# Kernel tuning notes

Measured on AMD Instinct MI355X. Metric: run time of the kernel, lower is better.

Reference implementation:

```python
import jax, jax.numpy as jnp
import numpy as np

PC_RANGE = (-50.0, -50.0, -4.0, 50.0, 50.0, 4.0)
IMG_H, IMG_W = 256.0, 704.0
EPS = 1e-5


def _bilinear_sample(feat, u, v):
    # feat [H,W,C]; u,v [M] in [0,1]; matches F.grid_sample(align_corners=False, padding_mode='zeros')
    H, W, _ = feat.shape
    x = u * W - 0.5
    y = v * H - 0.5
    x0 = jnp.floor(x)
    y0 = jnp.floor(y)
    dx = (x - x0)[:, None]
    dy = (y - y0)[:, None]
    x0 = x0.astype(jnp.int32)
    y0 = y0.astype(jnp.int32)

    def g(xi, yi):
        inb = ((xi >= 0) & (xi < W) & (yi >= 0) & (yi < H)).astype(feat.dtype)[:, None]
        return feat[jnp.clip(yi, 0, H - 1), jnp.clip(xi, 0, W - 1)] * inb

    return (g(x0, y0) * (1 - dx) * (1 - dy) + g(x0 + 1, y0) * dx * (1 - dy)
            + g(x0, y0 + 1) * (1 - dx) * dy + g(x0 + 1, y0 + 1) * dx * dy)


def _conv1x1(t, w, b):
    return jnp.einsum('bchw,oc->bohw', t, w) + b[None, :, None, None]


def _inorm(t, eps=1e-5):
    # InstanceNorm2d (affine=False): normalize per (b, c) over spatial dims
    m = t.mean(axis=(2, 3), keepdims=True)
    var = t.var(axis=(2, 3), keepdims=True)
    return (t - m) * jax.lax.rsqrt(var + eps)


def _forward(feat, lidar2img, bev_pos, pe_w1, pe_b1, pe_w2, pe_b2, pe_w3, pe_b3,
             c1_w, c1_b, c2_w, c2_b, c3_w, c3_b):
    B, N, C, Hf, Wf = feat.shape
    _, P, Hb, Wb, _ = bev_pos.shape
    Q = Hb * Wb
    lo = jnp.asarray(PC_RANGE[:3], feat.dtype)
    hi = jnp.asarray(PC_RANGE[3:], feat.dtype)
    # 'b p h w d -> b (h w) p d', then scale normalized coords into pc_range
    ref01 = jnp.transpose(bev_pos, (0, 2, 3, 1, 4)).reshape(B, Q, P, 3)
    ref = ref01 * (hi - lo) + lo
    # project through per-camera lidar2img (homogeneous)
    pts = jnp.concatenate([ref, jnp.ones_like(ref[..., :1])], axis=-1)  # [B,Q,P,4]
    cam = jnp.einsum('bnij,bqpj->bnqpi', lidar2img, pts)                # [B,N,Q,P,4]
    homo = cam[..., 2]
    z = jnp.maximum(homo, EPS)
    u = cam[..., 0] / z / IMG_W
    v = cam[..., 1] / z / IMG_H
    valid = ((homo > EPS) & (u > 0.0) & (u < 1.0) & (v > 0.0) & (v < 1.0)).astype(feat.dtype)
    # bilinear gather per camera; feats to channel-last ('b n (g c) h w -> (b g) n h w c', G=1)
    fmap = jnp.transpose(feat, (0, 1, 3, 4, 2)).reshape(B * N, Hf, Wf, C)
    samp = jax.vmap(_bilinear_sample)(fmap, u.reshape(B * N, Q * P), v.reshape(B * N, Q * P))
    samp = samp.reshape(B, N, Q, P, C) * valid[..., None]
    samp = samp.sum(axis=1)  # sum over cameras -> [B,Q,P,C]
    # PositionalEncodingMap(3 -> 256 -> 256 -> 128) on normalized reference points
    pe = jax.nn.relu(ref01 @ pe_w1 + pe_b1)
    pe = jax.nn.relu(pe @ pe_w2 + pe_b2)
    pe = pe @ pe_w3 + pe_b3
    samp = samp + pe
    # 'b (h w) g p c -> b (p g c) h w' with g=1
    x = jnp.transpose(samp.reshape(B, Hb, Wb, P, C), (0, 3, 4, 1, 2)).reshape(B, P * C, Hb, Wb)
    gelu = lambda t: jax.nn.gelu(t, approximate=False)
    x = gelu(_inorm(_conv1x1(x, c1_w, c1_b)))
    x = gelu(_inorm(_conv1x1(x, c2_w, c2_b)))
    x = _conv1x1(x, c3_w, c3_b)
    return x


def setup_inputs() -> dict:
    key = jax.random.key(0)
    ks = jax.random.split(key, 16)
    B, N, C, Hf, Wf = 1, 6, 128, 32, 88
    P, Hb, Wb = 4, 160, 160
    E = 128
    MID = 256
    s = 0.02
    return {
        'feat': jax.random.normal(ks[0], (B, N, C, Hf, Wf), jnp.float32),
        'lidar2img': jax.random.normal(ks[1], (B, N, 4, 4), jnp.float32),
        'bev_pos': jax.random.uniform(ks[2], (B, P, Hb, Wb, 3), jnp.float32),
        'pe_w1': jax.random.normal(ks[3], (3, MID), jnp.float32) * s,
        'pe_b1': jnp.zeros((MID,), jnp.float32),
        'pe_w2': jax.random.normal(ks[4], (MID, MID), jnp.float32) * s,
        'pe_b2': jnp.zeros((MID,), jnp.float32),
        'pe_w3': jax.random.normal(ks[5], (MID, E), jnp.float32) * s,
        'pe_b3': jnp.zeros((E,), jnp.float32),
        'c1_w': jax.random.normal(ks[6], (4 * E, P * 128), jnp.float32) * s,
        'c1_b': jnp.zeros((4 * E,), jnp.float32),
        'c2_w': jax.random.normal(ks[7], (E, 4 * E), jnp.float32) * s,
        'c2_b': jnp.zeros((E,), jnp.float32),
        'c3_w': jax.random.normal(ks[8], (E, E), jnp.float32) * s,
        'c3_b': jnp.zeros((E,), jnp.float32),
    }


def reference(feat, lidar2img, bev_pos, pe_w1, pe_b1, pe_w2, pe_b2, pe_w3, pe_b3,
              c1_w, c1_b, c2_w, c2_b, c3_w, c3_b):
    return _forward(feat, lidar2img, bev_pos, pe_w1, pe_b1, pe_w2, pe_b2, pe_w3, pe_b3,
                    c1_w, c1_b, c2_w, c2_b, c3_w, c3_b)
```

## Files before the change

### kernel.cpp

```cpp
#include <hip/hip_runtime.h>
#include <cstdint>
#include <cstddef>

using frag8 = __attribute__((ext_vector_type(8))) short;
using f32x4 = __attribute__((ext_vector_type(4))) float;

__device__ __forceinline__ float b2f_bits(unsigned short u) {
    union { uint32_t u32; float f; } x; x.u32 = ((uint32_t)u) << 16; return x.f;
}
__device__ __forceinline__ float b2f_lo(uint32_t pk) {
    return __builtin_bit_cast(float, pk << 16);
}
__device__ __forceinline__ float b2f_hi(uint32_t pk) {
    return __builtin_bit_cast(float, pk & 0xffff0000u);
}
__device__ __forceinline__ unsigned short f2b(float f) {
    uint32_t u = __builtin_bit_cast(uint32_t, f);
    uint32_t r = (u + 0x7fffu + ((u >> 16) & 1u)) >> 16;
    return (unsigned short)r;
}

#define HF 32
#define WFEAT 88
#define NCAM 6
#define NPT 102400
#define BM 128
#define BN 128
#define BK 64

__global__ void k_transpose_feat(const float* __restrict__ feat,
                                 unsigned short* __restrict__ featT) {
    int idx = blockIdx.x * 256 + threadIdx.x;
    if (idx >= NCAM * 128 * HF * WFEAT) return;
    int c = idx & 127;
    int rest = idx >> 7;
    int x = rest % WFEAT; rest /= WFEAT;
    int y = rest % HF;
    int n = rest / HF;
    featT[idx] = f2b(feat[((n * 128 + c) * HF + y) * WFEAT + x]);
}

__global__ void k_transpose_w(const float* __restrict__ w,
                              unsigned short* __restrict__ wt, int R, int C) {
    int idx = blockIdx.x * 256 + threadIdx.x;
    if (idx >= R * C) return;
    int r = idx / C, c = idx - r * C;
    wt[c * R + r] = f2b(w[idx]);
}

__global__ void k_cast(const float* __restrict__ w, unsigned short* __restrict__ wb, int n) {
    int idx = blockIdx.x * 256 + threadIdx.x;
    if (idx < n) wb[idx] = f2b(w[idx]);
}

__global__ __launch_bounds__(256) void k_project(const float* __restrict__ l2i,
                                                 const float* __restrict__ bev,
                                                 int* __restrict__ poff,
                                                 float4* __restrict__ pwts) {
    int idx = blockIdx.x * 256 + threadIdx.x;
    if (idx >= NCAM * NPT) return;
    int n = idx / NPT, pt = idx - n * NPT;
    int q = pt >> 2, p = pt & 3;
    int h = q / 160, w = q - h * 160;
    const float* bv = bev + ((p * 160 + h) * 160 + w) * 3;
    float rx = bv[0] * 100.f - 50.f;
    float ry = bv[1] * 100.f - 50.f;
    float rz = bv[2] * 8.f - 4.f;
    const float* M = l2i + n * 16;
    float c0   = M[0] * rx + M[1] * ry + M[2]  * rz + M[3];
    float c1v  = M[4] * rx + M[5] * ry + M[6]  * rz + M[7];
    float homo = M[8] * rx + M[9] * ry + M[10] * rz + M[11];
    float z = fmaxf(homo, 1e-5f);
    float u = c0 / z / 704.0f;
    float v = c1v / z / 256.0f;
    if (!(homo > 1e-5f && u > 0.f && u < 1.f && v > 0.f && v < 1.f)) {
        poff[idx] = -1;
        return;
    }
    float fx = u * (float)WFEAT - 0.5f;
    float fy = v * (float)HF - 0.5f;
    float fx0 = floorf(fx), fy0 = floorf(fy);
    float dx = fx - fx0, dy = fy - fy0;
    int x0 = (int)fx0, y0 = (int)fy0;
    float wxa = (x0 < 0) ? dx : 1.f - dx;
    float wxb = (x0 >= 0 && x0 < WFEAT - 1) ? dx : 0.f;
    float wya = (y0 < 0) ? dy : 1.f - dy;
    float wyb = (y0 >= 0 && y0 < HF - 1) ? dy : 0.f;
    int bx = max(x0, 0), by = max(y0, 0);
    poff[idx] = ((n * HF + by) * WFEAT + bx) << 7;
    pwts[idx] = make_float4(wxa * wya, wxb * wya, wxa * wyb, wxb * wyb);
}

__global__ __launch_bounds__(256) void k_sample2(const unsigned short* __restrict__ featT,
                                                 const int* __restrict__ poff,
                                                 const float4* __restrict__ pwts,
                                                 unsigned short* __restrict__ samp) {
    int pt = blockIdx.x * 4 + (threadIdx.x >> 6);
    int lane = threadIdx.x & 63;
    int c2 = lane * 2;
    int offs[NCAM];
    float4 ww[NCAM];
    #pragma unroll
    for (int n = 0; n < NCAM; ++n) offs[n] = poff[n * NPT + pt];
    #pragma unroll
    for (int n = 0; n < NCAM; ++n) ww[n] = pwts[n * NPT + pt];
    float acc0 = 0.f, acc1 = 0.f;
    #pragma unroll
    for (int n = 0; n < NCAM; ++n) {
        if (offs[n] >= 0) {
            const unsigned short* base = featT + offs[n] + c2;
            uint32_t p00 = *(const uint32_t*)(base);
            uint32_t p01 = *(const uint32_t*)(base + 128);
            uint32_t p10 = *(const uint32_t*)(base + WFEAT * 128);
            uint32_t p11 = *(const uint32_t*)(base + WFEAT * 128 + 128);
            float4 w = ww[n];
            acc0 += w.x * b2f_lo(p00) + w.y * b2f_lo(p01) + w.z * b2f_lo(p10) + w.w * b2f_lo(p11);
            acc1 += w.x * b2f_hi(p00) + w.y * b2f_hi(p01) + w.z * b2f_hi(p10) + w.w * b2f_hi(p11);
        }
    }
    uint32_t outpk = (uint32_t)f2b(acc0) | ((uint32_t)f2b(acc1) << 16);
    *(uint32_t*)(samp + (size_t)pt * 128 + c2) = outpk;
}

__global__ __launch_bounds__(256) void k_pe1(const float* __restrict__ bev,
                                             const float* __restrict__ w1,
                                             const float* __restrict__ b1,
                                             unsigned short* __restrict__ H1) {
    int idx = blockIdx.x * 256 + threadIdx.x;
    int m = idx >> 6;
    int o4 = (idx & 63) * 4;
    int q = m >> 2, p = m & 3;
    int h = q / 160, w = q - h * 160;
    const float* bv = bev + ((p * 160 + h) * 160 + w) * 3;
    float cx = bv[0], cy = bv[1], cz = bv[2];
    float4 a0 = *(const float4*)(w1 + o4);
    float4 a1 = *(const float4*)(w1 + 256 + o4);
    float4 a2 = *(const float4*)(w1 + 512 + o4);
    float4 bb = *(const float4*)(b1 + o4);
    ushort4 o;
    o.x = f2b(fmaxf(cx * a0.x + cy * a1.x + cz * a2.x + bb.x, 0.f));
    o.y = f2b(fmaxf(cx * a0.y + cy * a1.y + cz * a2.y + bb.y, 0.f));
    o.z = f2b(fmaxf(cx * a0.z + cy * a1.z + cz * a2.z + bb.z, 0.f));
    o.w = f2b(fmaxf(cx * a0.w + cy * a1.w + cz * a2.w + bb.w, 0.f));
    *(ushort4*)(H1 + (size_t)m * 256 + o4) = o;
}

__device__ __forceinline__ void stage_tile(const unsigned short* __restrict__ g, int ld,
                                           unsigned short* lds, int wave, int lane) {
    #pragma unroll
    for (int j = 0; j < 4; ++j) {
        int idx = wave * 256 + j * 64 + lane;
        int r = idx >> 3;
        int cs = idx & 7;
        int cl = cs ^ (r & 7);
        __builtin_amdgcn_global_load_lds(
            (const __attribute__((address_space(1))) void*)(g + (size_t)r * ld + cl * 8),
            (__attribute__((address_space(3))) void*)(lds + wave * 2048 + j * 512),
            16, 0, 0);
    }
}

__device__ __forceinline__ frag8 frag_read(const unsigned short* lds, int row, int chunk) {
    return *(const frag8*)(lds + row * 64 + ((chunk ^ (row & 7)) << 3));
}

__device__ __forceinline__ void mma_tile(const unsigned short* As, const unsigned short* Bs,
                                         int wm, int wn, int lane, f32x4 (&acc)[4][4]) {
    int lm = lane & 15, lq = lane >> 4;
    #pragma unroll
    for (int kk = 0; kk < 2; ++kk) {
        frag8 a[4], b[4];
        #pragma unroll
        for (int t = 0; t < 4; ++t) a[t] = frag_read(As, wm * 64 + t * 16 + lm, kk * 4 + lq);
        #pragma unroll
        for (int t = 0; t < 4; ++t) b[t] = frag_read(Bs, wn * 64 + t * 16 + lm, kk * 4 + lq);
        #pragma unroll
        for (int tm = 0; tm < 4; ++tm)
            #pragma unroll
            for (int tn = 0; tn < 4; ++tn)
                acc[tm][tn] = __builtin_amdgcn_mfma_f32_16x16x32_bf16(a[tm], b[tn], acc[tm][tn], 0, 0, 0);
    }
}

__global__ __launch_bounds__(256) void k_gemm_pe2(const unsigned short* __restrict__ A,
                                                  const unsigned short* __restrict__ Bt,
                                                  const float* __restrict__ bias,
                                                  unsigned short* __restrict__ H2) {
    __shared__ unsigned short As[BM * BK], Bs[BN * BK];
    int lane = threadIdx.x & 63, wave = threadIdx.x >> 6;
    int wm = wave >> 1, wn = wave & 1;
    int m0 = blockIdx.x * BM, n0 = blockIdx.y * BN;
    f32x4 acc[4][4] = {};
    for (int kt = 0; kt < 4; ++kt) {
        stage_tile(A + (size_t)m0 * 256 + kt * BK, 256, As, wave, lane);
        stage_tile(Bt + (size_t)n0 * 256 + kt * BK, 256, Bs, wave, lane);
        __syncthreads();
        mma_tile(As, Bs, wm, wn, lane, acc);
        __syncthreads();
    }
    int lm = lane & 15, lq = lane >> 4;
    #pragma unroll
    for (int tn = 0; tn < 4; ++tn) {
        int n = n0 + wn * 64 + tn * 16 + lm;
        float bn = bias[n];
        #pragma unroll
        for (int tm = 0; tm < 4; ++tm) {
            int mb = m0 + wm * 64 + tm * 16 + lq * 4;
            #pragma unroll
            for (int rr = 0; rr < 4; ++rr)
                H2[(size_t)(mb + rr) * 256 + n] = f2b(fmaxf(acc[tm][tn][rr] + bn, 0.f));
        }
    }
}

__global__ __launch_bounds__(256) void k_gemm_pe3(const unsigned short* __restrict__ A,
                                                  const unsigned short* __restrict__ Bt,
                                                  const float* __restrict__ bias,
                                                  const unsigned short* __restrict__ samp,
                                                  unsigned short* __restrict__ X) {
    __shared__ unsigned short As[BM * BK], Bs[BN * BK];
    int lane = threadIdx.x & 63, wave = threadIdx.x >> 6;
    int wm = wave >> 1, wn = wave & 1;
    int m0 = blockIdx.x * BM;
    f32x4 acc[4][4] = {};
    for (int kt = 0; kt < 4; ++kt) {
        stage_tile(A + (size_t)m0 * 256 + kt * BK, 256, As, wave, lane);
        stage_tile(Bt + (size_t)kt * BK, 256, Bs, wave, lane);
        __syncthreads();
        mma_tile(As, Bs, wm, wn, lane, acc);
        __syncthreads();
    }
    int lm = lane & 15, lq = lane >> 4;
    #pragma unroll
    for (int tn = 0; tn < 4; ++tn) {
        int n = wn * 64 + tn * 16 + lm;
        float bn = bias[n];
        #pragma unroll
        for (int tm = 0; tm < 4; ++tm) {
            int mb = m0 + wm * 64 + tm * 16 + lq * 4;
            #pragma unroll
            for (int rr = 0; rr < 4; ++rr) {
                size_t off = (size_t)(mb + rr) * 128 + n;
                X[off] = f2b(acc[tm][tn][rr] + bn + b2f_bits(samp[off]));
            }
        }
    }
}

template <int K, bool STATS>
__global__ __launch_bounds__(256) void k_gemm_conv(const unsigned short* __restrict__ A,
                                                   const unsigned short* __restrict__ Bt,
                                                   const float* __restrict__ bias,
                                                   unsigned short* __restrict__ Y, int ldY,
                                                   float* __restrict__ st, int C) {
    __shared__ unsigned short As[BM * BK], Bs[BN * BK];
    int lane = threadIdx.x & 63, wave = threadIdx.x >> 6;
    int wm = wave >> 1, wn = wave & 1;
    int m0 = blockIdx.x * BM, n0 = blockIdx.y * BN;
    f32x4 acc[4][4] = {};
    for (int kt = 0; kt < K / BK; ++kt) {
        stage_tile(A + (size_t)m0 * K + kt * BK, K, As, wave, lane);
        stage_tile(Bt + (size_t)n0 * K + kt * BK, K, Bs, wave, lane);
        __syncthreads();
        mma_tile(As, Bs, wm, wn, lane, acc);
        __syncthreads();
    }
    int lm = lane & 15, lq = lane >> 4;
    #pragma unroll
    for (int tn = 0; tn < 4; ++tn) {
        int n = n0 + wn * 64 + tn * 16 + lm;
        float bn = bias[n];
        float s1 = 0.f, s2 = 0.f;
        #pragma unroll
        for (int tm = 0; tm < 4; ++tm) {
            int mb = m0 + wm * 64 + tm * 16 + lq * 4;
            #pragma unroll
            for (int rr = 0; rr < 4; ++rr) {
                float v = acc[tm][tn][rr] + bn;
                Y[(size_t)(mb + rr) * ldY + n] = f2b(v);
                if (STATS) { s1 += v; s2 += v * v; }
            }
        }
        if (STATS) {
            s1 += __shfl_xor(s1, 16); s1 += __shfl_xor(s1, 32);
            s2 += __shfl_xor(s2, 16); s2 += __shfl_xor(s2, 32);
            if (lq == 0) { atomicAdd(&st[n], s1); atomicAdd(&st[C + n], s2); }
        }
    }
}

__global__ __launch_bounds__(256) void k_gemm_conv3(const unsigned short* __restrict__ A,
                                                    const unsigned short* __restrict__ Bt,
                                                    const float* __restrict__ bias,
                                                    float* __restrict__ out) {
    __shared__ unsigned short As[BM * BK], Bs[BN * BK];
    int lane = threadIdx.x & 63, wave = threadIdx.x >> 6;
    int wm = wave >> 1, wn = wave & 1;
    int m0 = blockIdx.x * BM;
    f32x4 acc[4][4] = {};
    for (int kt = 0; kt < 2; ++kt) {
        stage_tile(A + (size_t)m0 * 128 + kt * BK, 128, As, wave, lane);
        stage_tile(Bt + (size_t)kt * BK, 128, Bs, wave, lane);
        __syncthreads();
        mma_tile(As, Bs, wm, wn, lane, acc);
        __syncthreads();
    }
    int lm = lane & 15, lq = lane >> 4;
    #pragma unroll
    for (int tn = 0; tn < 4; ++tn) {
        int n = wn * 64 + tn * 16 + lm;
        float bn = bias[n];
        #pragma unroll
        for (int tm = 0; tm < 4; ++tm) {
            int mb = m0 + wm * 64 + tm * 16 + lq * 4;
            float4 pk;
            pk.x = acc[tm][tn][0] + bn;
            pk.y = acc[tm][tn][1] + bn;
            pk.z = acc[tm][tn][2] + bn;
            pk.w = acc[tm][tn][3] + bn;
            *(float4*)(out + (size_t)n * 25600 + mb) = pk;
        }
    }
}

__global__ void k_finalize(const float* __restrict__ st, float* __restrict__ ms,
                           int C, float inv_n) {
    int c = blockIdx.x * 256 + threadIdx.x;
    if (c >= C) return;
    float mean = st[c] * inv_n;
    float var = st[C + c] * inv_n - mean * mean;
    ms[c] = mean;
    ms[C + c] = rsqrtf(var + 1e-5f);
}

__global__ void k_normgelu8(const unsigned short* __restrict__ Y, const float* __restrict__ ms,
                            unsigned short* __restrict__ X2, int Cmask, int C, int total8) {
    int i8 = blockIdx.x * 256 + threadIdx.x;
    if (i8 >= total8) return;
    int e0 = i8 * 8;
    int c = e0 & Cmask;
    uint4 y = *(const uint4*)(Y + e0);
    const float is2 = 0.70710678118654752f;
    unsigned int yw[4] = {y.x, y.y, y.z, y.w};
    unsigned int ow[4];
    #pragma unroll
    for (int j = 0; j < 4; ++j) {
        float2 mu = *(const float2*)(ms + c + j * 2);
        float2 rs = *(const float2*)(ms + C + c + j * 2);
        float v0 = (b2f_bits((unsigned short)(yw[j] & 0xffffu)) - mu.x) * rs.x;
        float v1 = (b2f_bits((unsigned short)(yw[j] >> 16)) - mu.y) * rs.y;
        float g0 = 0.5f * v0 * (1.f + erff(v0 * is2));
        float g1 = 0.5f * v1 * (1.f + erff(v1 * is2));
        ow[j] = (uint32_t)f2b(g0) | ((uint32_t)f2b(g1) << 16);
    }
    *(uint4*)(X2 + e0) = make_uint4(ow[0], ow[1], ow[2], ow[3]);
}

extern "C" void kernel_launch(void* const* d_in, const int* in_sizes, int n_in,
                              void* d_out, int out_size, void* d_ws, size_t ws_size,
                              hipStream_t stream) {
    (void)in_sizes; (void)n_in; (void)out_size; (void)ws_size;
    const float* feat = (const float*)d_in[0];
    const float* l2i  = (const float*)d_in[1];
    const float* bev  = (const float*)d_in[2];
    const float* pw1  = (const float*)d_in[3];
    const float* pb1  = (const float*)d_in[4];
    const float* pw2  = (const float*)d_in[5];
    const float* pb2  = (const float*)d_in[6];
    const float* pw3  = (const float*)d_in[7];
    const float* pb3  = (const float*)d_in[8];
    const float* c1w  = (const float*)d_in[9];
    const float* c1b  = (const float*)d_in[10];
    const float* c2w  = (const float*)d_in[11];
    const float* c2b  = (const float*)d_in[12];
    const float* c3w  = (const float*)d_in[13];
    const float* c3b  = (const float*)d_in[14];
    float* outp = (float*)d_out;
    char* ws = (char*)d_ws;

    unsigned short* featT = (unsigned short*)(ws + 0);
    unsigned short* W2Tb  = (unsigned short*)(ws + 4348416);
    unsigned short* W3Tb  = (unsigned short*)(ws + 4479488);
    unsigned short* C1Wb  = (unsigned short*)(ws + 4545024);
    unsigned short* C2Wb  = (unsigned short*)(ws + 5069312);
    unsigned short* C3Wb  = (unsigned short*)(ws + 5200384);
    float* stats          = (float*)(ws + 5233152);
    int*    poff          = (int*)(ws + 5243392);
    float4* pwts          = (float4*)(ws + 7700992);
    char* BUF1 = ws + 17531392;
    char* BUF2 = ws + 69960192;
    char* BUF3 = ws + 122388992;

    float* st512 = stats;
    float* ms512 = stats + 1024;
    float* st128 = stats + 2048;
    float* ms128 = stats + 2304;

    unsigned short* H1   = (unsigned short*)BUF1;
    unsigned short* H2   = (unsigned short*)BUF2;
    unsigned short* samp = (unsigned short*)BUF3;
    unsigned short* X    = (unsigned short*)BUF1;
    unsigned short* Y1   = (unsigned short*)BUF2;
    unsigned short* X2   = (unsigned short*)BUF3;
    unsigned short* Y2   = (unsigned short*)BUF1;
    unsigned short* X3   = (unsigned short*)(BUF1 + 6553600);

    k_transpose_feat<<<8448, 256, 0, stream>>>(feat, featT);
    k_transpose_w<<<256, 256, 0, stream>>>(pw2, W2Tb, 256, 256);
    k_transpose_w<<<128, 256, 0, stream>>>(pw3, W3Tb, 256, 128);
    k_cast<<<1024, 256, 0, stream>>>(c1w, C1Wb, 262144);
    k_cast<<<256, 256, 0, stream>>>(c2w, C2Wb, 65536);
    k_cast<<<64, 256, 0, stream>>>(c3w, C3Wb, 16384);
    hipMemsetAsync(stats, 0, 10240, stream);

    k_project<<<2400, 256, 0, stream>>>(l2i, bev, poff, pwts);
    k_sample2<<<25600, 256, 0, stream>>>(featT, poff, pwts, samp);

    k_pe1<<<25600, 256, 0, stream>>>(bev, pw1, pb1, H1);
    k_gemm_pe2<<<dim3(800, 2), 256, 0, stream>>>(H1, W2Tb, pb2, H2);
    k_gemm_pe3<<<dim3(800, 1), 256, 0, stream>>>(H2, W3Tb, pb3, samp, X);

    k_gemm_conv<512, true><<<dim3(200, 4), 256, 0, stream>>>(X, C1Wb, c1b, Y1, 512, st512, 512);
    k_finalize<<<2, 256, 0, stream>>>(st512, ms512, 512, 1.f / 25600.f);
    k_normgelu8<<<6400, 256, 0, stream>>>(Y1, ms512, X2, 511, 512, 1638400);

    k_gemm_conv<512, true><<<dim3(200, 1), 256, 0, stream>>>(X2, C2Wb, c2b, Y2, 128, st128, 128);
    k_finalize<<<1, 256, 0, stream>>>(st128, ms128, 128, 1.f / 25600.f);
    k_normgelu8<<<1600, 256, 0, stream>>>(Y2, ms128, X3, 127, 128, 409600);

    k_gemm_conv3<<<dim3(200, 1), 256, 0, stream>>>(X3, C3Wb, c3b, outp);
}
```

Measured before the change: 309.7 us.

## Double-buffer LDS tiles in all MFMA GEMM kernels

Replaces the single-buffered load/sync/compute/sync loop in the four GEMM kernels with a shared double-buffered loop. The next K-tile is staged into the alternate LDS buffer while MFMAs run on the current one, and one barrier per iteration is removed. This doubles LDS use per block, which may lower occupancy, and the K loops are short (2 to a few iterations), so there is little to overlap.

Result: slower. 321.4 us (+3.8%).

```diff
diff --git a/kernel.cpp b/kernel.cpp
--- a/kernel.cpp
+++ b/kernel.cpp
@@ -182,22 +182,39 @@
     }
 }
 
+template <int KT>
+__device__ __forceinline__ void gemm_loop_db(const unsigned short* __restrict__ A, int ldA,
+                                             const unsigned short* __restrict__ B, int ldB,
+                                             unsigned short (*As)[BM * BK],
+                                             unsigned short (*Bs)[BN * BK],
+                                             int wave, int lane, int wm, int wn,
+                                             f32x4 (&acc)[4][4]) {
+    stage_tile(A, ldA, As[0], wave, lane);
+    stage_tile(B, ldB, Bs[0], wave, lane);
+    __syncthreads();
+    #pragma unroll
+    for (int kt = 0; kt < KT; ++kt) {
+        int cur = kt & 1, nxt = cur ^ 1;
+        if (kt + 1 < KT) {
+            stage_tile(A + (kt + 1) * BK, ldA, As[nxt], wave, lane);
+            stage_tile(B + (kt + 1) * BK, ldB, Bs[nxt], wave, lane);
+        }
+        mma_tile(As[cur], Bs[cur], wm, wn, lane, acc);
+        __syncthreads();
+    }
+}
+
 __global__ __launch_bounds__(256) void k_gemm_pe2(const unsigned short* __restrict__ A,
                                                   const unsigned short* __restrict__ Bt,
                                                   const float* __restrict__ bias,
                                                   unsigned short* __restrict__ H2) {
-    __shared__ unsigned short As[BM * BK], Bs[BN * BK];
+    __shared__ unsigned short As[2][BM * BK], Bs[2][BN * BK];
     int lane = threadIdx.x & 63, wave = threadIdx.x >> 6;
     int wm = wave >> 1, wn = wave & 1;
     int m0 = blockIdx.x * BM, n0 = blockIdx.y * BN;
     f32x4 acc[4][4] = {};
-    for (int kt = 0; kt < 4; ++kt) {
-        stage_tile(A + (size_t)m0 * 256 + kt * BK, 256, As, wave, lane);
-        stage_tile(Bt + (size_t)n0 * 256 + kt * BK, 256, Bs, wave, lane);
-        __syncthreads();
-        mma_tile(As, Bs, wm, wn, lane, acc);
-        __syncthreads();
-    }
+    gemm_loop_db<4>(A + (size_t)m0 * 256, 256, Bt + (size_t)n0 * 256, 256,
+                    As, Bs, wave, lane, wm, wn, acc);
     int lm = lane & 15, lq = lane >> 4;
     #pragma unroll
     for (int tn = 0; tn < 4; ++tn) {
@@ -218,18 +235,13 @@
                                                   const float* __restrict__ bias,
                                                   const unsigned short* __restrict__ samp,
                                                   unsigned short* __restrict__ X) {
-    __shared__ unsigned short As[BM * BK], Bs[BN * BK];
+    __shared__ unsigned short As[2][BM * BK], Bs[2][BN * BK];
     int lane = threadIdx.x & 63, wave = threadIdx.x >> 6;
     int wm = wave >> 1, wn = wave & 1;
     int m0 = blockIdx.x * BM;
     f32x4 acc[4][4] = {};
-    for (int kt = 0; kt < 4; ++kt) {
-        stage_tile(A + (size_t)m0 * 256 + kt * BK, 256, As, wave, lane);
-        stage_tile(Bt + (size_t)kt * BK, 256, Bs, wave, lane);
-        __syncthreads();
-        mma_tile(As, Bs, wm, wn, lane, acc);
-        __syncthreads();
-    }
+    gemm_loop_db<4>(A + (size_t)m0 * 256, 256, Bt, 256,
+                    As, Bs, wave, lane, wm, wn, acc);
     int lm = lane & 15, lq = lane >> 4;
     #pragma unroll
     for (int tn = 0; tn < 4; ++tn) {
@@ -253,18 +265,13 @@
                                                    const float* __restrict__ bias,
                                                    unsigned short* __restrict__ Y, int ldY,
                                                    float* __restrict__ st, int C) {
-    __shared__ unsigned short As[BM * BK], Bs[BN * BK];
+    __shared__ unsigned short As[2][BM * BK], Bs[2][BN * BK];
     int lane = threadIdx.x & 63, wave = threadIdx.x >> 6;
     int wm = wave >> 1, wn = wave & 1;
     int m0 = blockIdx.x * BM, n0 = blockIdx.y * BN;
     f32x4 acc[4][4] = {};
-    for (int kt = 0; kt < K / BK; ++kt) {
-        stage_tile(A + (size_t)m0 * K + kt * BK, K, As, wave, lane);
-        stage_tile(Bt + (size_t)n0 * K + kt * BK, K, Bs, wave, lane);
-        __syncthreads();
-        mma_tile(As, Bs, wm, wn, lane, acc);
-        __syncthreads();
-    }
+    gemm_loop_db<K / BK>(A + (size_t)m0 * K, K, Bt + (size_t)n0 * K, K,
+                         As, Bs, wave, lane, wm, wn, acc);
     int lm = lane & 15, lq = lane >> 4;
     #pragma unroll
     for (int tn = 0; tn < 4; ++tn) {
@@ -293,18 +300,13 @@
                                                     const unsigned short* __restrict__ Bt,
                                                     const float* __restrict__ bias,
                                                     float* __restrict__ out) {
-    __shared__ unsigned short As[BM * BK], Bs[BN * BK];
+    __shared__ unsigned short As[2][BM * BK], Bs[2][BN * BK];
     int lane = threadIdx.x & 63, wave = threadIdx.x >> 6;
     int wm = wave >> 1, wn = wave & 1;
     int m0 = blockIdx.x * BM;
     f32x4 acc[4][4] = {};
-    for (int kt = 0; kt < 2; ++kt) {
-        stage_tile(A + (size_t)m0 * 128 + kt * BK, 128, As, wave, lane);
-        stage_tile(Bt + (size_t)kt * BK, 128, Bs, wave, lane);
-        __syncthreads();
-        mma_tile(As, Bs, wm, wn, lane, acc);
-        __syncthreads();
-    }
+    gemm_loop_db<2>(A + (size_t)m0 * 128, 128, Bt, 128,
+                    As, Bs, wave, lane, wm, wn, acc);
     int lm = lane & 15, lq = lane >> 4;
     #pragma unroll
     for (int tn = 0; tn < 4; ++tn) {
```

## Use 256x256 double-buffered 1024-thread GEMM tiles for pe2 and conv1

Applied to the files above, without the earlier changes.

Replaces the 128x128 tile, 256-thread GEMMs for the second positional-encoding layer and the first 1x1 conv with 256x256 tiles run by 16 waves per block. K is staged 32 at a time into double-buffered LDS with a new swizzle, so the load of the next slice overlaps the MFMA work on the current one. The larger tiles are meant to raise operand reuse and cut global traffic. In exchange, each block uses 64KB of LDS, fewer blocks run per CU, and there are far fewer blocks in the grid (400 and 200), which may leave CUs underfilled.

New measurement: 297.7 us. 1.04x faster.

```diff
diff --git a/kernel.cpp b/kernel.cpp
--- a/kernel.cpp
+++ b/kernel.cpp
@@ -145,6 +145,116 @@
     *(ushort4*)(H1 + (size_t)m * 256 + o4) = o;
 }
 
+__device__ __forceinline__ void stage_tile_big(const unsigned short* __restrict__ g, int ld,
+                                               unsigned short* lds, int t) {
+    int r = t >> 2, cs = t & 3;
+    int cl = cs ^ ((r >> 1) & 3);
+    __builtin_amdgcn_global_load_lds(
+        (const __attribute__((address_space(1))) void*)(g + (size_t)r * ld + cl * 8),
+        (__attribute__((address_space(3))) void*)(lds + (t >> 6) * 512),
+        16, 0, 0);
+}
+
+__device__ __forceinline__ frag8 frag_read_big(const unsigned short* lds, int row, int chunk) {
+    return *(const frag8*)(lds + row * 32 + ((chunk ^ ((row >> 1) & 3)) << 3));
+}
+
+__device__ __forceinline__ void mma_tile_big(const unsigned short* As, const unsigned short* Bs,
+                                             int wm, int wn, int lane, f32x4 (&acc)[4][4]) {
+    int lm = lane & 15, lq = lane >> 4;
+    frag8 a[4], b[4];
+    #pragma unroll
+    for (int t = 0; t < 4; ++t) a[t] = frag_read_big(As, wm * 64 + t * 16 + lm, lq);
+    #pragma unroll
+    for (int t = 0; t < 4; ++t) b[t] = frag_read_big(Bs, wn * 64 + t * 16 + lm, lq);
+    #pragma unroll
+    for (int tm = 0; tm < 4; ++tm)
+        #pragma unroll
+        for (int tn = 0; tn < 4; ++tn)
+            acc[tm][tn] = __builtin_amdgcn_mfma_f32_16x16x32_bf16(a[tm], b[tn], acc[tm][tn], 0, 0, 0);
+}
+
+template <int KT>
+__device__ __forceinline__ void gemm_loop_big(const unsigned short* __restrict__ A, int ldA,
+                                              const unsigned short* __restrict__ B, int ldB,
+                                              unsigned short (*As)[256 * 32],
+                                              unsigned short (*Bs)[256 * 32],
+                                              int t, int wm, int wn, int lane,
+                                              f32x4 (&acc)[4][4]) {
+    stage_tile_big(A, ldA, As[0], t);
+    stage_tile_big(B, ldB, Bs[0], t);
+    __syncthreads();
+    #pragma unroll
+    for (int kt = 0; kt < KT; ++kt) {
+        int cur = kt & 1, nxt = cur ^ 1;
+        if (kt + 1 < KT) {
+            stage_tile_big(A + (kt + 1) * 32, ldA, As[nxt], t);
+            stage_tile_big(B + (kt + 1) * 32, ldB, Bs[nxt], t);
+        }
+        mma_tile_big(As[cur], Bs[cur], wm, wn, lane, acc);
+        __syncthreads();
+    }
+}
+
+__global__ __launch_bounds__(1024) void k_gemm_pe2_big(const unsigned short* __restrict__ A,
+                                                       const unsigned short* __restrict__ Bt,
+                                                       const float* __restrict__ bias,
+                                                       unsigned short* __restrict__ H2) {
+    __shared__ unsigned short As[2][256 * 32], Bs[2][256 * 32];
+    int t = threadIdx.x, lane = t & 63, wid = t >> 6;
+    int wm = wid >> 2, wn = wid & 3;
+    int m0 = blockIdx.x * 256;
+    f32x4 acc[4][4] = {};
+    gemm_loop_big<8>(A + (size_t)m0 * 256, 256, Bt, 256, As, Bs, t, wm, wn, lane, acc);
+    int lm = lane & 15, lq = lane >> 4;
+    #pragma unroll
+    for (int tn = 0; tn < 4; ++tn) {
+        int n = wn * 64 + tn * 16 + lm;
+        float bn = bias[n];
+        #pragma unroll
+        for (int tm = 0; tm < 4; ++tm) {
+            int mb = m0 + wm * 64 + tm * 16 + lq * 4;
+            #pragma unroll
+            for (int rr = 0; rr < 4; ++rr)
+                H2[(size_t)(mb + rr) * 256 + n] = f2b(fmaxf(acc[tm][tn][rr] + bn, 0.f));
+        }
+    }
+}
+
+__global__ __launch_bounds__(1024) void k_gemm_conv1_big(const unsigned short* __restrict__ A,
+                                                         const unsigned short* __restrict__ Bt,
+                                                         const float* __restrict__ bias,
+                                                         unsigned short* __restrict__ Y,
+                                                         float* __restrict__ st) {
+    __shared__ unsigned short As[2][256 * 32], Bs[2][256 * 32];
+    int t = threadIdx.x, lane = t & 63, wid = t >> 6;
+    int wm = wid >> 2, wn = wid & 3;
+    int m0 = blockIdx.x * 256, n0 = blockIdx.y * 256;
+    f32x4 acc[4][4] = {};
+    gemm_loop_big<16>(A + (size_t)m0 * 512, 512, Bt + (size_t)n0 * 512, 512,
+                      As, Bs, t, wm, wn, lane, acc);
+    int lm = lane & 15, lq = lane >> 4;
+    #pragma unroll
+    for (int tn = 0; tn < 4; ++tn) {
+        int n = n0 + wn * 64 + tn * 16 + lm;
+        float bn = bias[n];
+        float s1 = 0.f, s2 = 0.f;
+        #pragma unroll
+        for (int tm = 0; tm < 4; ++tm) {
+            int mb = m0 + wm * 64 + tm * 16 + lq * 4;
+            #pragma unroll
+            for (int rr = 0; rr < 4; ++rr) {
+                float v = acc[tm][tn][rr] + bn;
+                Y[(size_t)(mb + rr) * 512 + n] = f2b(v);
+                s1 += v; s2 += v * v;
+            }
+        }
+        s1 += __shfl_xor(s1, 16); s1 += __shfl_xor(s1, 32);
+        s2 += __shfl_xor(s2, 16); s2 += __shfl_xor(s2, 32);
+        if (lq == 0) { atomicAdd(&st[n], s1); atomicAdd(&st[512 + n], s2); }
+    }
+}
+
 __device__ __forceinline__ void stage_tile(const unsigned short* __restrict__ g, int ld,
                                            unsigned short* lds, int wave, int lane) {
     #pragma unroll
@@ -179,37 +289,6 @@
             #pragma unroll
             for (int tn = 0; tn < 4; ++tn)
                 acc[tm][tn] = __builtin_amdgcn_mfma_f32_16x16x32_bf16(a[tm], b[tn], acc[tm][tn], 0, 0, 0);
-    }
-}
-
-__global__ __launch_bounds__(256) void k_gemm_pe2(const unsigned short* __restrict__ A,
-                                                  const unsigned short* __restrict__ Bt,
-                                                  const float* __restrict__ bias,
-                                                  unsigned short* __restrict__ H2) {
-    __shared__ unsigned short As[BM * BK], Bs[BN * BK];
-    int lane = threadIdx.x & 63, wave = threadIdx.x >> 6;
-    int wm = wave >> 1, wn = wave & 1;
-    int m0 = blockIdx.x * BM, n0 = blockIdx.y * BN;
-    f32x4 acc[4][4] = {};
-    for (int kt = 0; kt < 4; ++kt) {
-        stage_tile(A + (size_t)m0 * 256 + kt * BK, 256, As, wave, lane);
-        stage_tile(Bt + (size_t)n0 * 256 + kt * BK, 256, Bs, wave, lane);
-        __syncthreads();
-        mma_tile(As, Bs, wm, wn, lane, acc);
-        __syncthreads();
-    }
-    int lm = lane & 15, lq = lane >> 4;
-    #pragma unroll
-    for (int tn = 0; tn < 4; ++tn) {
-        int n = n0 + wn * 64 + tn * 16 + lm;
-        float bn = bias[n];
-        #pragma unroll
-        for (int tm = 0; tm < 4; ++tm) {
-            int mb = m0 + wm * 64 + tm * 16 + lq * 4;
-            #pragma unroll
-            for (int rr = 0; rr < 4; ++rr)
-                H2[(size_t)(mb + rr) * 256 + n] = f2b(fmaxf(acc[tm][tn][rr] + bn, 0.f));
-        }
     }
 }
 
@@ -417,10 +496,10 @@
     k_sample2<<<25600, 256, 0, stream>>>(featT, poff, pwts, samp);
 
     k_pe1<<<25600, 256, 0, stream>>>(bev, pw1, pb1, H1);
-    k_gemm_pe2<<<dim3(800, 2), 256, 0, stream>>>(H1, W2Tb, pb2, H2);
+    k_gemm_pe2_big<<<400, 1024, 0, stream>>>(H1, W2Tb, pb2, H2);
     k_gemm_pe3<<<dim3(800, 1), 256, 0, stream>>>(H2, W3Tb, pb3, samp, X);
 
-    k_gemm_conv<512, true><<<dim3(200, 4), 256, 0, stream>>>(X, C1Wb, c1b, Y1, 512, st512, 512);
+    k_gemm_conv1_big<<<dim3(100, 2), 1024, 0, stream>>>(X, C1Wb, c1b, Y1, st512);
     k_finalize<<<2, 256, 0, stream>>>(st512, ms512, 512, 1.f / 25600.f);
     k_normgelu8<<<6400, 256, 0, stream>>>(Y1, ms512, X2, 511, 512, 1638400);
 
```
